# Optimization experiments

Hardware: AMD Instinct MI355X
Metric: run time of the kernel (lower is better)

## Reference

```python
import jax, jax.numpy as jnp
import numpy as np

B = 4096           # batch size
NG = 4096          # num_gene_sets (columns of input)
G = 1024           # number of aggregation groups
GS = 32            # members per group (CSR-packed; code handles ragged too)
T = G * GS         # total flat indices


def setup_inputs() -> dict:
    key = jax.random.key(0)
    k1, k2, k3 = jax.random.split(key, 3)
    gene_set_features = jax.random.normal(k1, (B, NG), dtype=jnp.float32)
    att_weights = jax.random.normal(k2, (T,), dtype=jnp.float32)  # concat of per-group logits
    flat_idx = jax.random.randint(k3, (T,), 0, NG, dtype=jnp.int64)
    segment_ids = (jnp.arange(T, dtype=jnp.int64) // GS)          # sorted group id per entry
    return {
        "gene_set_features": gene_set_features,
        "att_weights": att_weights,
        "flat_idx": flat_idx,
        "segment_ids": segment_ids,
        "num_segments": G,
    }


def reference(gene_set_features, att_weights, flat_idx, segment_ids, num_segments):
    # Per-group (segment) softmax over the batch-independent attention logits.
    seg_max = jax.ops.segment_max(att_weights, segment_ids, num_segments=num_segments)
    ex = jnp.exp(att_weights - seg_max[segment_ids])
    denom = jax.ops.segment_sum(ex, segment_ids, num_segments=num_segments)
    attn = ex / denom[segment_ids]                     # (T,) softmax weights per group
    # Gather all group members for every batch row in one shot, weight, segment-sum.
    gathered = gene_set_features[:, flat_idx]          # (B, T)
    weighted = gathered * attn[None, :]                # (B, T)
    out = jax.ops.segment_sum(weighted.T, segment_ids, num_segments=num_segments).T  # (B, G)
    return out
```

## Files before the change

### kernel.cpp

```cpp
#include <hip/hip_runtime.h>

#define NGK 4096
#define BK 4096
#define GK 1024
#define GSK 32
#define TK (GK * GSK)

#define BTILE 8
#define AGG_THREADS 512

__device__ __forceinline__ unsigned pack2bf16(float a, float b) {
    unsigned ua = __float_as_uint(a);
    unsigned ub = __float_as_uint(b);
    ua = (ua + 0x7fffu + ((ua >> 16) & 1u)) >> 16;
    ub = (ub + 0x7fffu + ((ub >> 16) & 1u)) >> 16;
    return ua | (ub << 16);
}

__global__ __launch_bounds__(256) void seg_softmax_kernel(
        const float* __restrict__ att,
        const int*   __restrict__ idx,
        unsigned*    __restrict__ pairs) {
    int t = blockIdx.x * 256 + threadIdx.x;
    float w = att[t];

    float m = w;
    #pragma unroll
    for (int d = 16; d >= 1; d >>= 1) m = fmaxf(m, __shfl_xor(m, d, 32));
    float e = expf(w - m);
    float s = e;
    #pragma unroll
    for (int d = 16; d >= 1; d >>= 1) s += __shfl_xor(s, d, 32);

    unsigned uw = __float_as_uint(e / s);
    uw = (uw + 0x7fffu + ((uw >> 16) & 1u)) & 0xffff0000u;

    int g = t >> 5;
    int j = t & 31;
    pairs[((j >> 2) * GK + g) * 4 + (j & 3)] = uw | (unsigned)idx[t];
}

__global__ __launch_bounds__(AGG_THREADS, 4) void stage_probe_kernel(
        const float* __restrict__ F,
        unsigned*    __restrict__ dummy) {
    __shared__ uint4 lds4[NGK];
    const int tid = threadIdx.x;
    const int b0 = blockIdx.x * BTILE;

    #pragma unroll
    for (int it = 0; it < NGK / AGG_THREADS; ++it) {
        int c = tid + it * AGG_THREADS;
        uint4 q;
        q.x = pack2bf16(F[(b0 + 0) * NGK + c], F[(b0 + 1) * NGK + c]);
        q.y = pack2bf16(F[(b0 + 2) * NGK + c], F[(b0 + 3) * NGK + c]);
        q.z = pack2bf16(F[(b0 + 4) * NGK + c], F[(b0 + 5) * NGK + c]);
        q.w = pack2bf16(F[(b0 + 6) * NGK + c], F[(b0 + 7) * NGK + c]);
        lds4[c] = q;
    }
    __syncthreads();

    unsigned v = 0;
    #pragma unroll
    for (int it = 0; it < NGK / AGG_THREADS; ++it)
        v ^= lds4[tid + it * AGG_THREADS].x;
    dummy[blockIdx.x * AGG_THREADS + tid] = v;
}

__global__ __launch_bounds__(AGG_THREADS, 4) void agg_kernel(
        const float* __restrict__ F,
        const uint4* __restrict__ pairs4,
        float*       __restrict__ out) {
    __shared__ uint4 lds4[NGK];

    const int tid = threadIdx.x;
    const int b0 = blockIdx.x * BTILE;

    #pragma unroll
    for (int it = 0; it < NGK / AGG_THREADS; ++it) {
        int c = tid + it * AGG_THREADS;
        uint4 q;
        q.x = pack2bf16(F[(b0 + 0) * NGK + c], F[(b0 + 1) * NGK + c]);
        q.y = pack2bf16(F[(b0 + 2) * NGK + c], F[(b0 + 3) * NGK + c]);
        q.z = pack2bf16(F[(b0 + 4) * NGK + c], F[(b0 + 5) * NGK + c]);
        q.w = pack2bf16(F[(b0 + 6) * NGK + c], F[(b0 + 7) * NGK + c]);
        lds4[c] = q;
    }
    __syncthreads();

    const char* ldsb = reinterpret_cast<const char*>(lds4);

    #pragma unroll
    for (int k = 0; k < GK / AGG_THREADS; ++k) {
        int g = tid + k * AGG_THREADS;
        float a0 = 0.f, a1 = 0.f, a2 = 0.f, a3 = 0.f;
        float a4 = 0.f, a5 = 0.f, a6 = 0.f, a7 = 0.f;
        #pragma unroll 2
        for (int jj = 0; jj < GSK / 4; ++jj) {
            uint4 u = pairs4[jj * GK + g];
            #pragma unroll
            for (int c = 0; c < 4; ++c) {
                unsigned uc = (c == 0) ? u.x : (c == 1) ? u.y : (c == 2) ? u.z : u.w;
                uint4 q = *reinterpret_cast<const uint4*>(ldsb + ((uc & 0xfffu) << 4));
                float w = __uint_as_float(uc & 0xffff0000u);
                a0 += w * __uint_as_float(q.x << 16);
                a1 += w * __uint_as_float(q.x & 0xffff0000u);
                a2 += w * __uint_as_float(q.y << 16);
                a3 += w * __uint_as_float(q.y & 0xffff0000u);
                a4 += w * __uint_as_float(q.z << 16);
                a5 += w * __uint_as_float(q.z & 0xffff0000u);
                a6 += w * __uint_as_float(q.w << 16);
                a7 += w * __uint_as_float(q.w & 0xffff0000u);
            }
        }
        out[(b0 + 0) * GK + g] = a0;
        out[(b0 + 1) * GK + g] = a1;
        out[(b0 + 2) * GK + g] = a2;
        out[(b0 + 3) * GK + g] = a3;
        out[(b0 + 4) * GK + g] = a4;
        out[(b0 + 5) * GK + g] = a5;
        out[(b0 + 6) * GK + g] = a6;
        out[(b0 + 7) * GK + g] = a7;
    }
}

extern "C" void kernel_launch(void* const* d_in, const int* in_sizes, int n_in,
                              void* d_out, int out_size, void* d_ws, size_t ws_size,
                              hipStream_t stream) {
    const float* F   = (const float*)d_in[0];
    const float* att = (const float*)d_in[1];
    const int*   idx = (const int*)d_in[2];

    unsigned* pairs = (unsigned*)d_ws;
    unsigned* dummy = (unsigned*)((char*)d_ws + (1 << 20));
    float*    out   = (float*)d_out;

    seg_softmax_kernel<<<TK / 256, 256, 0, stream>>>(att, idx, pairs);
    stage_probe_kernel<<<BK / BTILE, AGG_THREADS, 0, stream>>>(F, dummy);
    agg_kernel<<<BK / BTILE, AGG_THREADS, 0, stream>>>(F, (const uint4*)pairs, out);
}
```

Before: 124.9 us.

## Drop staging probe kernel and split aggregation into two half-batch phases

Removes the diagnostic stage_probe_kernel, which re-read the full feature matrix and wrote dummy output. The aggregation kernel now stages the first four batch rows into LDS and holds the other four in registers, so those global loads are in flight during the first gather phase. A second phase then packs and aggregates the remaining rows. This adds a second sync and a second pass over the pair list, and raises register pressure from the 32 buffered floats per thread plus full unrolling.

```diff
diff --git a/kernel.cpp b/kernel.cpp
--- a/kernel.cpp
+++ b/kernel.cpp
@@ -40,37 +40,12 @@
     pairs[((j >> 2) * GK + g) * 4 + (j & 3)] = uw | (unsigned)idx[t];
 }
 
-__global__ __launch_bounds__(AGG_THREADS, 4) void stage_probe_kernel(
-        const float* __restrict__ F,
-        unsigned*    __restrict__ dummy) {
-    __shared__ uint4 lds4[NGK];
-    const int tid = threadIdx.x;
-    const int b0 = blockIdx.x * BTILE;
-
-    #pragma unroll
-    for (int it = 0; it < NGK / AGG_THREADS; ++it) {
-        int c = tid + it * AGG_THREADS;
-        uint4 q;
-        q.x = pack2bf16(F[(b0 + 0) * NGK + c], F[(b0 + 1) * NGK + c]);
-        q.y = pack2bf16(F[(b0 + 2) * NGK + c], F[(b0 + 3) * NGK + c]);
-        q.z = pack2bf16(F[(b0 + 4) * NGK + c], F[(b0 + 5) * NGK + c]);
-        q.w = pack2bf16(F[(b0 + 6) * NGK + c], F[(b0 + 7) * NGK + c]);
-        lds4[c] = q;
-    }
-    __syncthreads();
-
-    unsigned v = 0;
-    #pragma unroll
-    for (int it = 0; it < NGK / AGG_THREADS; ++it)
-        v ^= lds4[tid + it * AGG_THREADS].x;
-    dummy[blockIdx.x * AGG_THREADS + tid] = v;
-}
-
 __global__ __launch_bounds__(AGG_THREADS, 4) void agg_kernel(
         const float* __restrict__ F,
         const uint4* __restrict__ pairs4,
         float*       __restrict__ out) {
-    __shared__ uint4 lds4[NGK];
+    __shared__ uint2 ldsA[NGK];
+    __shared__ uint2 ldsB[NGK];
 
     const int tid = threadIdx.x;
     const int b0 = blockIdx.x * BTILE;
@@ -78,44 +53,78 @@
     #pragma unroll
     for (int it = 0; it < NGK / AGG_THREADS; ++it) {
         int c = tid + it * AGG_THREADS;
-        uint4 q;
+        uint2 q;
         q.x = pack2bf16(F[(b0 + 0) * NGK + c], F[(b0 + 1) * NGK + c]);
         q.y = pack2bf16(F[(b0 + 2) * NGK + c], F[(b0 + 3) * NGK + c]);
-        q.z = pack2bf16(F[(b0 + 4) * NGK + c], F[(b0 + 5) * NGK + c]);
-        q.w = pack2bf16(F[(b0 + 6) * NGK + c], F[(b0 + 7) * NGK + c]);
-        lds4[c] = q;
+        ldsA[c] = q;
+    }
+
+    float fb[NGK / AGG_THREADS][4];
+    #pragma unroll
+    for (int it = 0; it < NGK / AGG_THREADS; ++it) {
+        int c = tid + it * AGG_THREADS;
+        fb[it][0] = F[(b0 + 4) * NGK + c];
+        fb[it][1] = F[(b0 + 5) * NGK + c];
+        fb[it][2] = F[(b0 + 6) * NGK + c];
+        fb[it][3] = F[(b0 + 7) * NGK + c];
     }
     __syncthreads();
 
-    const char* ldsb = reinterpret_cast<const char*>(lds4);
+    const char* ldsbA = reinterpret_cast<const char*>(ldsA);
+    const char* ldsbB = reinterpret_cast<const char*>(ldsB);
 
     #pragma unroll
     for (int k = 0; k < GK / AGG_THREADS; ++k) {
         int g = tid + k * AGG_THREADS;
         float a0 = 0.f, a1 = 0.f, a2 = 0.f, a3 = 0.f;
-        float a4 = 0.f, a5 = 0.f, a6 = 0.f, a7 = 0.f;
-        #pragma unroll 2
+        #pragma unroll
         for (int jj = 0; jj < GSK / 4; ++jj) {
             uint4 u = pairs4[jj * GK + g];
             #pragma unroll
             for (int c = 0; c < 4; ++c) {
                 unsigned uc = (c == 0) ? u.x : (c == 1) ? u.y : (c == 2) ? u.z : u.w;
-                uint4 q = *reinterpret_cast<const uint4*>(ldsb + ((uc & 0xfffu) << 4));
+                uint2 q = *reinterpret_cast<const uint2*>(ldsbA + ((uc & 0xfffu) << 3));
                 float w = __uint_as_float(uc & 0xffff0000u);
                 a0 += w * __uint_as_float(q.x << 16);
                 a1 += w * __uint_as_float(q.x & 0xffff0000u);
                 a2 += w * __uint_as_float(q.y << 16);
                 a3 += w * __uint_as_float(q.y & 0xffff0000u);
-                a4 += w * __uint_as_float(q.z << 16);
-                a5 += w * __uint_as_float(q.z & 0xffff0000u);
-                a6 += w * __uint_as_float(q.w << 16);
-                a7 += w * __uint_as_float(q.w & 0xffff0000u);
             }
         }
         out[(b0 + 0) * GK + g] = a0;
         out[(b0 + 1) * GK + g] = a1;
         out[(b0 + 2) * GK + g] = a2;
         out[(b0 + 3) * GK + g] = a3;
+    }
+
+    #pragma unroll
+    for (int it = 0; it < NGK / AGG_THREADS; ++it) {
+        int c = tid + it * AGG_THREADS;
+        uint2 q;
+        q.x = pack2bf16(fb[it][0], fb[it][1]);
+        q.y = pack2bf16(fb[it][2], fb[it][3]);
+        ldsB[c] = q;
+    }
+    __syncthreads();
+
+    #pragma unroll
+    for (int k = 0; k < GK / AGG_THREADS; ++k) {
+        int g = tid + k * AGG_THREADS;
+        float a4 = 0.f, a5 = 0.f, a6 = 0.f, a7 = 0.f;
+        #pragma unroll
+        for (int jj = 0; jj < GSK / 4; ++jj) {
+            uint4 u = pairs4[jj * GK + g];
+            #pragma unroll
+            for (int c = 0; c < 4; ++c) {
+                unsigned uc = (c == 0) ? u.x : (c == 1) ? u.y : (c == 2) ? u.z : u.w;
+                uint2 q = *reinterpret_cast<const uint2*>(ldsbB + ((uc & 0xfffu) << 3));
+                float w = __uint_as_float(uc & 0xffff0000u);
+                a4 += w * __uint_as_float(q.x << 16);
+                a5 += w * __uint_as_float(q.x & 0xffff0000u);
+                a6 += w * __uint_as_float(q.y << 16);
+                a7 += w * __uint_as_float(q.y & 0xffff0000u);
+            }
+        }
         out[(b0 + 4) * GK + g] = a4;
         out[(b0 + 5) * GK + g] = a5;
         out[(b0 + 6) * GK + g] = a6;
@@ -131,10 +140,8 @@
     const int*   idx = (const int*)d_in[2];
 
     unsigned* pairs = (unsigned*)d_ws;
-    unsigned* dummy = (unsigned*)((char*)d_ws + (1 << 20));
     float*    out   = (float*)d_out;
 
     seg_softmax_kernel<<<TK / 256, 256, 0, stream>>>(att, idx, pairs);
-    stage_probe_kernel<<<BK / BTILE, AGG_THREADS, 0, stream>>>(F, dummy);
     agg_kernel<<<BK / BTILE, AGG_THREADS, 0, stream>>>(F, (const uint4*)pairs, out);
 }
```

After: 151.4 us. 1.21x slower.
